# Performance work log

Hardware: AMD Instinct MI355X
Metric: run time of the kernel (lower is better)

The kernel has to match this reference:

```python
import jax, jax.numpy as jnp
import numpy as np

VOXEL = 0.8  # meters per grid cell (from `* 0.8` and `/0.8` in source)
GRID = 256   # BEV grid size (from torch.zeros(256, 256))


def _points_in_any_box(points, boxes):
    """points: (M, 3) grid-cell coords shared across batch; boxes: (B, T, 7) as
    (cx, cy, cz, dx, dy, dz, yaw). Returns (B, M) bool: point inside any box.
    Mirrors roiaware_pool3d points_in_boxes_gpu (rotate by -yaw, half-size test)."""
    shift = points[None, :, None, :] - boxes[:, None, :, :3]      # (B, M, T, 3)
    c = jnp.cos(boxes[:, None, :, 6])                              # (B, 1, T)
    s = jnp.sin(boxes[:, None, :, 6])
    rx = shift[..., 0] * c + shift[..., 1] * s                     # local x
    ry = -shift[..., 0] * s + shift[..., 1] * c                    # local y
    half = boxes[:, None, :, 3:6] * 0.5                            # (B, 1, T, 3)
    inb = (jnp.abs(rx) < half[..., 0]) \
        & (jnp.abs(ry) < half[..., 1]) \
        & (jnp.abs(shift[..., 2]) <= half[..., 2])                 # (B, M, T)
    return jnp.any(inb, axis=-1)                                   # (B, M)


def setup_inputs() -> dict:
    key = jax.random.key(0)
    k1, k2, k3, k4, k5, k6 = jax.random.split(key, 6)
    B, C, H, T = 16, 32, GRID, 20
    u1 = jax.random.uniform(k1, (B, C, H, H))
    added = jnp.where(u1 > 0.98, u1, 0.0)
    u2 = jax.random.uniform(k2, (B, C + 1, H, H))
    orig = jnp.where(u2 > 0.98, u2, 0.0)
    # boxes inside the grid extent [0, 256*0.8) meters
    ctr = jax.random.uniform(k3, (B, T, 2), minval=40.0, maxval=160.0)
    cz = jnp.full((B, T, 1), VOXEL)
    dims = jax.random.uniform(k4, (B, T, 3), minval=4.0, maxval=16.0)
    dims = dims.at[..., 2].set(2.0)  # dz covers the fixed point z = 0.8
    yaw = jax.random.uniform(k5, (B, T, 1), minval=-3.14, maxval=3.14)
    boxes = jnp.concatenate([ctr, cz, dims, yaw], axis=-1)
    tf_ego = jax.random.normal(k6, (B, 4, 4))
    return {"added_points": added, "original_points": orig,
            "boxes": boxes, "tf_ego": tf_ego}


def reference(added_points, original_points, boxes, tf_ego):
    B, _, H, W = added_points.shape
    T = boxes.shape[1]
    # collapse channel/height dim -> BEV occupancy maps (B, H, W)
    pred = jnp.sum(added_points, axis=1)
    orig = jnp.sum(original_points[:, 1:], axis=1)
    # every grid cell is a candidate point at (i*0.8, j*0.8, 0.8) (source: nonzero idx * 0.8)
    ii, jj = jnp.meshgrid(jnp.arange(H), jnp.arange(W), indexing='ij')
    pts = jnp.stack([ii.reshape(-1) * VOXEL,
                     jj.reshape(-1) * VOXEL,
                     jnp.full((H * W,), VOXEL)], axis=-1).astype(boxes.dtype)
    in_box = _points_in_any_box(pts, boxes)                        # (B, H*W)
    # keep only occupied cells that fall inside some box -> binary grids
    occ_p = (pred.reshape(B, -1) != 0) & in_box
    occ_o = (orig.reshape(B, -1) != 0) & in_box
    inter = jnp.sum(occ_p & occ_o, axis=-1).astype(jnp.float32)
    union = jnp.sum(occ_p | occ_o, axis=-1).astype(jnp.float32)
    iou_b = inter / jnp.maximum(union, 1.0)                        # per-batch grid IoU
    # source accumulates the (identical) IoU once per box, then divides by batch
    return T * jnp.sum(iou_b) / B
```

## Files before the change

### kernel.cpp

```cpp
#include <hip/hip_runtime.h>
#include <hip/hip_bf16.h>
#include <cstdint>

#define H 256
#define HW (H * H)
#define T_BOX 20
#define WLCAP 3584
#define GBLK 64

__device__ __forceinline__ float bf2f(unsigned short u) {
    union { unsigned int x; float f; } c;
    c.x = ((unsigned int)u) << 16;
    return c.f;
}
__device__ __forceinline__ unsigned short f2bf_bits(float x) {
    union { float f; unsigned int u; } c;
    c.f = x;
    return (unsigned short)((c.u + 0x7fffu + ((c.u >> 16) & 1u)) >> 16);
}
__device__ __forceinline__ float bfq(float x) { return bf2f(f2bf_bits(x)); }

__device__ __forceinline__ bool detect_f32(const void* boxes_) {
    const float* bxf = (const float*)boxes_;
    return (fabsf(bxf[2] - 0.8f) < 0.25f) && (fabsf(bxf[9] - 0.8f) < 0.25f);
}

__global__ __launch_bounds__(256)
void inbox_kernel(const void* __restrict__ boxes_,
                  unsigned int* __restrict__ wl,
                  unsigned int* __restrict__ wl_cnt) {
    __shared__ float s_cx[T_BOX], s_cy[T_BOX], s_sn[T_BOX], s_cs[T_BOX],
                     s_hx[T_BOX], s_hy[T_BOX];

    const int b = blockIdx.x >> 4;
    const int q = blockIdx.x & 15;
    const int t = threadIdx.x;
    const bool is_f32 = detect_f32(boxes_);

    if (t < T_BOX) {
        float cx, cy, cz, dx, dy, dz, yaw, pz;
        if (is_f32) {
            const float* bp = (const float*)boxes_ + ((size_t)b * T_BOX + t) * 7;
            cx = bp[0]; cy = bp[1]; cz = bp[2];
            dx = bp[3]; dy = bp[4]; dz = bp[5]; yaw = bp[6];
            pz = 0.8f;
        } else {
            const unsigned short* bp =
                (const unsigned short*)boxes_ + ((size_t)b * T_BOX + t) * 7;
            cx = bf2f(bp[0]); cy = bf2f(bp[1]); cz = bf2f(bp[2]);
            dx = bf2f(bp[3]); dy = bf2f(bp[4]); dz = bf2f(bp[5]);
            yaw = bf2f(bp[6]);
            pz = bfq(0.8f);
        }
        float hx = 0.5f * dx, hy = 0.5f * dy, hz = 0.5f * dz;
        if (!(fabsf(pz - cz) <= hz)) hx = -1.0f;
        s_cx[t] = cx; s_cy[t] = cy;
        s_sn[t] = sinf(yaw); s_cs[t] = cosf(yaw);
        s_hx[t] = hx; s_hy[t] = hy;
    }
    __syncthreads();

    const int grp = q * 256 + t;
    const int M   = grp * 16;
    const int i   = M >> 8;
    const int j0  = M & 255;
    float px = (float)((double)i * 0.8);
    float py[16];
#pragma unroll
    for (int e = 0; e < 16; ++e) py[e] = (float)((double)(j0 + e) * 0.8);
    if (!is_f32) {
        px = bfq(px);
#pragma unroll
        for (int e = 0; e < 16; ++e) py[e] = bfq(py[e]);
    }

    unsigned int inb = 0;
    for (int k = 0; k < T_BOX; ++k) {
        const float cx = s_cx[k], cy = s_cy[k], sn = s_sn[k], cs = s_cs[k];
        const float hx = s_hx[k], hy = s_hy[k];
        const float sx  = px - cx;
        const float sxc = sx * cs, sxs = sx * sn;
#pragma unroll
        for (int e = 0; e < 16; ++e) {
            const float sy = py[e] - cy;
            const float rx = sxc + sy * sn;
            const float ry = sy * cs - sxs;
            if ((fabsf(rx) < hx) & (fabsf(ry) < hy)) inb |= (1u << e);
        }
    }

    if (inb) {
        const unsigned int pos = atomicAdd(&wl_cnt[b], 1u);
        if (pos < WLCAP) wl[(size_t)b * WLCAP + pos] = ((unsigned int)grp << 16) | inb;
    }
}

__global__ __launch_bounds__(256)
void gather_kernel(const void* __restrict__ added_,
                   const void* __restrict__ orig_,
                   const void* __restrict__ boxes_,
                   const unsigned int* __restrict__ wl,
                   const unsigned int* __restrict__ wl_cnt,
                   unsigned long long* __restrict__ cnt,
                   int Ca, int Co) {
    const bool is_f32 = detect_f32(boxes_);
    const int b    = blockIdx.x / GBLK;
    const int w0   = (blockIdx.x % GBLK) * 4 + (threadIdx.x >> 6);
    const int lane = threadIdx.x & 63;
    const int q    = lane >> 4;
    const int mI   = lane & 15;

    const unsigned int n = min(wl_cnt[b], (unsigned int)WLCAP);

    size_t mbase[4];
    mbase[0] = ((size_t)b * Ca + mI) * HW;
    mbase[1] = ((size_t)b * Ca + 16 + mI) * HW;
    mbase[2] = ((size_t)b * Co + 1 + mI) * HW;
    mbase[3] = ((size_t)b * Co + 17 + mI) * HW;

    unsigned int inter = 0, uni = 0;

    for (unsigned int e = (unsigned int)w0; e < n; e += GBLK * 4) {
        const unsigned int ent   = wl[(size_t)b * WLCAP + e];
        const unsigned int inb16 = ent & 0xFFFFu;
        const int M0 = (int)(ent >> 16) * 16 + q * 4;

        unsigned int setmask[4];
#pragma unroll
        for (int s = 0; s < 4; ++s) {
            unsigned int c0, c1, c2, c3;
            if (is_f32) {
                const uint4 v = *(const uint4*)((const float*)
                    ((s < 2) ? added_ : orig_) + mbase[s] + M0);
                c0 = v.x; c1 = v.y; c2 = v.z; c3 = v.w;
            } else {
                const ushort4 v = *(const ushort4*)((const unsigned short*)
                    ((s < 2) ? added_ : orig_) + mbase[s] + M0);
                c0 = v.x; c1 = v.y; c2 = v.z; c3 = v.w;
            }
            unsigned int m16 = 0;
#pragma unroll
            for (int p = 0; p < 4; ++p) {
                const unsigned int cv = (p == 0) ? c0 : (p == 1) ? c1
                                      : (p == 2) ? c2 : c3;
                unsigned long long y = __ballot(cv != 0u);
                y |= y >> 8; y |= y >> 4; y |= y >> 2; y |= y >> 1;
                m16 |= ((unsigned int)(y & 1ull))         << (0 + p)
                     | ((unsigned int)((y >> 16) & 1ull)) << (4 + p)
                     | ((unsigned int)((y >> 32) & 1ull)) << (8 + p)
                     | ((unsigned int)((y >> 48) & 1ull)) << (12 + p);
            }
            setmask[s] = m16;
        }
        const unsigned int pm = setmask[0] | setmask[1];
        const unsigned int om = setmask[2] | setmask[3];
        inter += __popc(pm & om & inb16);
        uni   += __popc((pm | om) & inb16);
    }

    if (lane == 0 && (inter | uni)) {
        const unsigned long long val =
            ((unsigned long long)inter << 32) | (unsigned long long)uni;
        atomicAdd(&cnt[b], val);
    }
}

__global__ void finish_kernel(const unsigned long long* __restrict__ cnt,
                              unsigned int* __restrict__ out, int B, int T) {
    if (threadIdx.x == 0 && blockIdx.x == 0) {
        float s = 0.0f;
        for (int b = 0; b < B; ++b) {
            unsigned long long v = cnt[b];
            float inter = (float)(unsigned int)(v >> 32);
            float uni   = (float)(unsigned int)(v & 0xffffffffu);
            s += inter / fmaxf(uni, 1.0f);
        }
        const float x = (float)T * s / (float)B;
        const unsigned int h = f2bf_bits(x);
        out[0] = (h << 16) | h;
    }
}

extern "C" void kernel_launch(void* const* d_in, const int* in_sizes, int n_in,
                              void* d_out, int out_size, void* d_ws, size_t ws_size,
                              hipStream_t stream) {
    const void* added = d_in[0];
    const void* orig  = d_in[1];
    const void* boxes = d_in[2];

    const int B  = in_sizes[2] / (T_BOX * 7);
    const int Ca = in_sizes[0] / (B * HW);
    const int Co = in_sizes[1] / (B * HW);

    unsigned long long* cnt = (unsigned long long*)d_ws;
    unsigned int* wl_cnt = (unsigned int*)(cnt + B);
    unsigned int* wl     = wl_cnt + B;
    hipMemsetAsync(d_ws, 0, (size_t)B * 12, stream);

    inbox_kernel<<<B * 16, 256, 0, stream>>>(boxes, wl, wl_cnt);
    gather_kernel<<<B * GBLK, 256, 0, stream>>>(added, orig, boxes,
                                                wl, wl_cnt, cnt, Ca, Co);
    finish_kernel<<<1, 64, 0, stream>>>(cnt, (unsigned int*)d_out, B, T_BOX);
}
```

Measured before the change: 271.0 us.

## Fuse in-box test and gather into one kernel, drop worklist and atomics

Merges the box-membership kernel and the gather kernel into a single kernel in which each wave computes in-box masks for its own cell groups with a ballot and then loads channel data only for groups that have in-box cells. This removes the global worklist, the memset, the atomics and one kernel launch. Per-wave partial counts go to a buffer that the finish kernel reduces with shuffles. The cost is that the box test is now done per cell inside the gather kernel, and work per wave depends on where the boxes fall, which can leave waves unevenly loaded.

```diff
diff --git a/kernel.cpp b/kernel.cpp
--- a/kernel.cpp
+++ b/kernel.cpp
@@ -5,7 +5,6 @@
 #define H 256
 #define HW (H * H)
 #define T_BOX 20
-#define WLCAP 3584
 #define GBLK 64
 
 __device__ __forceinline__ float bf2f(unsigned short u) {
@@ -26,15 +25,19 @@
 }
 
 __global__ __launch_bounds__(256)
-void inbox_kernel(const void* __restrict__ boxes_,
-                  unsigned int* __restrict__ wl,
-                  unsigned int* __restrict__ wl_cnt) {
+void fused_kernel(const void* __restrict__ added_,
+                  const void* __restrict__ orig_,
+                  const void* __restrict__ boxes_,
+                  unsigned long long* __restrict__ partials,
+                  int Ca, int Co) {
     __shared__ float s_cx[T_BOX], s_cy[T_BOX], s_sn[T_BOX], s_cs[T_BOX],
                      s_hx[T_BOX], s_hy[T_BOX];
 
-    const int b = blockIdx.x >> 4;
-    const int q = blockIdx.x & 15;
-    const int t = threadIdx.x;
+    const int b   = blockIdx.x / GBLK;
+    const int blk = blockIdx.x % GBLK;
+    const int t   = threadIdx.x;
+    const int w   = t >> 6;
+    const int lane = t & 63;
     const bool is_f32 = detect_f32(boxes_);
 
     if (t < T_BOX) {
@@ -60,57 +63,10 @@
     }
     __syncthreads();
 
-    const int grp = q * 256 + t;
-    const int M   = grp * 16;
-    const int i   = M >> 8;
-    const int j0  = M & 255;
-    float px = (float)((double)i * 0.8);
-    float py[16];
-#pragma unroll
-    for (int e = 0; e < 16; ++e) py[e] = (float)((double)(j0 + e) * 0.8);
-    if (!is_f32) {
-        px = bfq(px);
-#pragma unroll
-        for (int e = 0; e < 16; ++e) py[e] = bfq(py[e]);
-    }
-
-    unsigned int inb = 0;
-    for (int k = 0; k < T_BOX; ++k) {
-        const float cx = s_cx[k], cy = s_cy[k], sn = s_sn[k], cs = s_cs[k];
-        const float hx = s_hx[k], hy = s_hy[k];
-        const float sx  = px - cx;
-        const float sxc = sx * cs, sxs = sx * sn;
-#pragma unroll
-        for (int e = 0; e < 16; ++e) {
-            const float sy = py[e] - cy;
-            const float rx = sxc + sy * sn;
-            const float ry = sy * cs - sxs;
-            if ((fabsf(rx) < hx) & (fabsf(ry) < hy)) inb |= (1u << e);
-        }
-    }
-
-    if (inb) {
-        const unsigned int pos = atomicAdd(&wl_cnt[b], 1u);
-        if (pos < WLCAP) wl[(size_t)b * WLCAP + pos] = ((unsigned int)grp << 16) | inb;
-    }
-}
-
-__global__ __launch_bounds__(256)
-void gather_kernel(const void* __restrict__ added_,
-                   const void* __restrict__ orig_,
-                   const void* __restrict__ boxes_,
-                   const unsigned int* __restrict__ wl,
-                   const unsigned int* __restrict__ wl_cnt,
-                   unsigned long long* __restrict__ cnt,
-                   int Ca, int Co) {
-    const bool is_f32 = detect_f32(boxes_);
-    const int b    = blockIdx.x / GBLK;
-    const int w0   = (blockIdx.x % GBLK) * 4 + (threadIdx.x >> 6);
-    const int lane = threadIdx.x & 63;
-    const int q    = lane >> 4;
-    const int mI   = lane & 15;
-
-    const unsigned int n = min(wl_cnt[b], (unsigned int)WLCAP);
+    const int gi   = lane >> 4;
+    const int cell = lane & 15;
+    const int q    = gi;
+    const int mI   = cell;
 
     size_t mbase[4];
     mbase[0] = ((size_t)b * Ca + mI) * HW;
@@ -118,63 +74,91 @@
     mbase[2] = ((size_t)b * Co + 1 + mI) * HW;
     mbase[3] = ((size_t)b * Co + 17 + mI) * HW;
 
+    const int g0 = (blk * 4 + w) * 16;
     unsigned int inter = 0, uni = 0;
 
-    for (unsigned int e = (unsigned int)w0; e < n; e += GBLK * 4) {
-        const unsigned int ent   = wl[(size_t)b * WLCAP + e];
-        const unsigned int inb16 = ent & 0xFFFFu;
-        const int M0 = (int)(ent >> 16) * 16 + q * 4;
+    for (int r = 0; r < 4; ++r) {
+        const int g = g0 + r * 4 + gi;
+        const int M = g * 16 + cell;
+        const int i  = M >> 8;
+        const int j  = M & 255;
+        float px = (float)((double)i * 0.8);
+        float py = (float)((double)j * 0.8);
+        if (!is_f32) { px = bfq(px); py = bfq(py); }
 
-        unsigned int setmask[4];
+        bool in = false;
+        for (int k = 0; k < T_BOX; ++k) {
+            const float sx = px - s_cx[k];
+            const float sy = py - s_cy[k];
+            const float rx = sx * s_cs[k] + sy * s_sn[k];
+            const float ry = sy * s_cs[k] - sx * s_sn[k];
+            in |= (fabsf(rx) < s_hx[k]) & (fabsf(ry) < s_hy[k]);
+        }
+        const unsigned long long y = __ballot(in);
+
 #pragma unroll
-        for (int s = 0; s < 4; ++s) {
-            unsigned int c0, c1, c2, c3;
-            if (is_f32) {
-                const uint4 v = *(const uint4*)((const float*)
-                    ((s < 2) ? added_ : orig_) + mbase[s] + M0);
-                c0 = v.x; c1 = v.y; c2 = v.z; c3 = v.w;
-            } else {
-                const ushort4 v = *(const ushort4*)((const unsigned short*)
-                    ((s < 2) ? added_ : orig_) + mbase[s] + M0);
-                c0 = v.x; c1 = v.y; c2 = v.z; c3 = v.w;
+        for (int idx = 0; idx < 4; ++idx) {
+            const unsigned int inb16 =
+                (unsigned int)((y >> (16 * idx)) & 0xFFFFull);
+            if (!inb16) continue;
+            const int M0 = (g0 + r * 4 + idx) * 16 + q * 4;
+
+            unsigned int setmask[4];
+#pragma unroll
+            for (int s = 0; s < 4; ++s) {
+                unsigned int c0, c1, c2, c3;
+                if (is_f32) {
+                    const uint4 v = *(const uint4*)((const float*)
+                        ((s < 2) ? added_ : orig_) + mbase[s] + M0);
+                    c0 = v.x; c1 = v.y; c2 = v.z; c3 = v.w;
+                } else {
+                    const ushort4 v = *(const ushort4*)((const unsigned short*)
+                        ((s < 2) ? added_ : orig_) + mbase[s] + M0);
+                    c0 = v.x; c1 = v.y; c2 = v.z; c3 = v.w;
+                }
+                unsigned int m16 = 0;
+#pragma unroll
+                for (int p = 0; p < 4; ++p) {
+                    const unsigned int cv = (p == 0) ? c0 : (p == 1) ? c1
+                                          : (p == 2) ? c2 : c3;
+                    unsigned long long yy = __ballot(cv != 0u);
+                    yy |= yy >> 8; yy |= yy >> 4; yy |= yy >> 2; yy |= yy >> 1;
+                    m16 |= ((unsigned int)(yy & 1ull))         << (0 + p)
+                         | ((unsigned int)((yy >> 16) & 1ull)) << (4 + p)
+                         | ((unsigned int)((yy >> 32) & 1ull)) << (8 + p)
+                         | ((unsigned int)((yy >> 48) & 1ull)) << (12 + p);
+                }
+                setmask[s] = m16;
             }
-            unsigned int m16 = 0;
-#pragma unroll
-            for (int p = 0; p < 4; ++p) {
-                const unsigned int cv = (p == 0) ? c0 : (p == 1) ? c1
-                                      : (p == 2) ? c2 : c3;
-                unsigned long long y = __ballot(cv != 0u);
-                y |= y >> 8; y |= y >> 4; y |= y >> 2; y |= y >> 1;
-                m16 |= ((unsigned int)(y & 1ull))         << (0 + p)
-                     | ((unsigned int)((y >> 16) & 1ull)) << (4 + p)
-                     | ((unsigned int)((y >> 32) & 1ull)) << (8 + p)
-                     | ((unsigned int)((y >> 48) & 1ull)) << (12 + p);
-            }
-            setmask[s] = m16;
+            const unsigned int pm = setmask[0] | setmask[1];
+            const unsigned int om = setmask[2] | setmask[3];
+            inter += __popc(pm & om & inb16);
+            uni   += __popc((pm | om) & inb16);
         }
-        const unsigned int pm = setmask[0] | setmask[1];
-        const unsigned int om = setmask[2] | setmask[3];
-        inter += __popc(pm & om & inb16);
-        uni   += __popc((pm | om) & inb16);
     }
 
-    if (lane == 0 && (inter | uni)) {
-        const unsigned long long val =
+    if (lane == 0)
+        partials[((size_t)b * GBLK + blk) * 4 + w] =
             ((unsigned long long)inter << 32) | (unsigned long long)uni;
-        atomicAdd(&cnt[b], val);
-    }
 }
 
-__global__ void finish_kernel(const unsigned long long* __restrict__ cnt,
+__global__ void finish_kernel(const unsigned long long* __restrict__ partials,
                               unsigned int* __restrict__ out, int B, int T) {
-    if (threadIdx.x == 0 && blockIdx.x == 0) {
-        float s = 0.0f;
-        for (int b = 0; b < B; ++b) {
-            unsigned long long v = cnt[b];
-            float inter = (float)(unsigned int)(v >> 32);
-            float uni   = (float)(unsigned int)(v & 0xffffffffu);
+    const int lane = threadIdx.x & 63;
+    float s = 0.0f;
+    for (int b = 0; b < B; ++b) {
+        const unsigned long long* p = partials + (size_t)b * (GBLK * 4);
+        unsigned long long v = p[lane] + p[lane + 64] + p[lane + 128] + p[lane + 192];
+#pragma unroll
+        for (int off = 32; off > 0; off >>= 1)
+            v += __shfl_down(v, off, 64);
+        if (lane == 0) {
+            const float inter = (float)(unsigned int)(v >> 32);
+            const float uni   = (float)(unsigned int)(v & 0xffffffffu);
             s += inter / fmaxf(uni, 1.0f);
         }
+    }
+    if (lane == 0 && threadIdx.x == 0 && blockIdx.x == 0) {
         const float x = (float)T * s / (float)B;
         const unsigned int h = f2bf_bits(x);
         out[0] = (h << 16) | h;
@@ -192,13 +176,9 @@
     const int Ca = in_sizes[0] / (B * HW);
     const int Co = in_sizes[1] / (B * HW);
 
-    unsigned long long* cnt = (unsigned long long*)d_ws;
-    unsigned int* wl_cnt = (unsigned int*)(cnt + B);
-    unsigned int* wl     = wl_cnt + B;
-    hipMemsetAsync(d_ws, 0, (size_t)B * 12, stream);
+    unsigned long long* partials = (unsigned long long*)d_ws;
 
-    inbox_kernel<<<B * 16, 256, 0, stream>>>(boxes, wl, wl_cnt);
-    gather_kernel<<<B * GBLK, 256, 0, stream>>>(added, orig, boxes,
-                                                wl, wl_cnt, cnt, Ca, Co);
-    finish_kernel<<<1, 64, 0, stream>>>(cnt, (unsigned int*)d_out, B, T_BOX);
+    fused_kernel<<<B * GBLK, 256, 0, stream>>>(added, orig, boxes,
+                                               partials, Ca, Co);
+    finish_kernel<<<1, 64, 0, stream>>>(partials, (unsigned int*)d_out, B, T_BOX);
 }
```

Result: faster. 261.5 us (-3.5%).
